# Kernel optimization log

Measured on AMD Instinct MI355X. Metric: run time of the kernel, lower is better.

Reference implementation:

```python
import jax, jax.numpy as jnp
import numpy as np
import math

B, L, C, Hh, Ww = 1, 16, 32, 64, 64
Wf = Ww // 2 + 1
R = 16
GROUPS = 4
MID = 4  # max(C//16, 4)
DT_REF = 1.0
INJ_K = 2.0
EPS = 1e-5


def _conv2d(x, w, b):
    y = jax.lax.conv_general_dilated(x, w, (1, 1), 'SAME',
                                     dimension_numbers=('NCHW', 'OIHW', 'NCHW'))
    return y + b[None, :, None, None]


def _adaptive_avg_w(x, out_w):
    # adaptive avg pool along last axis (torch AdaptiveAvgPool semantics)
    w_in = x.shape[-1]
    cs = jnp.concatenate([jnp.zeros(x.shape[:-1] + (1,), x.dtype), jnp.cumsum(x, -1)], -1)
    starts = np.floor(np.arange(out_w) * w_in / out_w).astype(np.int32)
    ends = np.ceil((np.arange(out_w) + 1) * w_in / out_w).astype(np.int32)
    num = cs[..., ends] - cs[..., starts]
    den = jnp.asarray(ends - starts, x.dtype)
    return num / den


def setup_inputs() -> dict:
    key = jax.random.key(0)
    ks = jax.random.split(key, 24)
    s = 0.05
    inp = {}
    inp['x'] = jax.random.normal(ks[0], (B, C, L, Hh, Ww), jnp.float32)
    inp['dt'] = jax.random.uniform(ks[1], (B, L), jnp.float32, 0.1, 1.0)
    inp['conv1_w'] = jax.random.normal(ks[2], (C, C, 3, 3), jnp.float32) * s
    inp['conv1_b'] = jnp.zeros((C,), jnp.float32)
    inp['conv2_w'] = jax.random.normal(ks[3], (C, C, 3, 3), jnp.float32) * s
    inp['conv2_b'] = jnp.zeros((C,), jnp.float32)
    inp['gfc_w'] = jax.random.normal(ks[4], (C, C), jnp.float32) * s
    inp['gfc_b'] = jnp.zeros((C,), jnp.float32)
    inp['head_w'] = jax.random.normal(ks[5], (C * R * 3, C), jnp.float32) * 0.02
    hb = np.zeros((C, R, 3), np.float32); hb[..., 0] = 1.0; hb[..., 2] = -5.0
    inp['head_b'] = jnp.asarray(hb.reshape(-1))
    inp['mix_w'] = jnp.eye(2 * R, dtype=jnp.float32) + jax.random.normal(ks[6], (2 * R, 2 * R), jnp.float32) * 0.02
    inp['mix_b'] = jnp.zeros((2 * R,), jnp.float32)
    inp['rank_scale'] = jnp.ones((R,), jnp.float32)
    inp['proj_w'] = jax.random.normal(ks[7], (1, R), jnp.float32) * s
    inp['proj_b'] = jnp.zeros((1,), jnp.float32)
    inp['pif_w'] = jax.random.normal(ks[8], (C, C), jnp.float32) * s  # 1x1x1 Conv3d
    inp['pif_b'] = jnp.zeros((C,), jnp.float32)
    inp['gn_w'] = jnp.ones((C,), jnp.float32)
    inp['gn_b'] = jnp.zeros((C,), jnp.float32)
    inp['g1_w'] = jax.random.normal(ks[9], (MID, C), jnp.float32) * s
    inp['g1_b'] = jnp.zeros((MID,), jnp.float32)
    inp['g2_w'] = jax.random.normal(ks[10], (C, MID), jnp.float32) * s
    inp['g2_b'] = jnp.zeros((C,), jnp.float32)
    return inp


def _forward(x, dt, conv1_w, conv1_b, conv2_w, conv2_b, gfc_w, gfc_b, head_w, head_b,
             mix_w, mix_b, rank_scale, proj_w, proj_b, pif_w, pif_b, gn_w, gn_b,
             g1_w, g1_b, g2_w, g2_b):
    Bx, Cx, Lx, H, W = x.shape
    x_seq = jnp.transpose(x, (0, 2, 1, 3, 4))  # [B,L,C,H,W]
    # ---- DynamicsParameterEstimator on flattened [B*L,C,H,W] ----
    xf = x_seq.reshape(Bx * Lx, Cx, H, W)
    f = jax.nn.silu(_conv2d(xf, conv1_w, conv1_b))
    f = jax.nn.silu(_conv2d(f, conv2_w, conv2_b))
    glob = jax.nn.sigmoid(f.mean((2, 3)) @ gfc_w.T + gfc_b)  # [BL,C]
    f = f * glob[:, :, None, None]
    f = _adaptive_avg_w(f.mean(2), Wf)         # [BL,C,Wf]
    feat = jnp.transpose(f, (0, 2, 1))          # [BL,Wf,C]
    p = (feat @ head_w.T + head_b).reshape(Bx * Lx, Wf, Cx, R, 3)
    nu = jax.nn.softplus(p[..., 0]).reshape(Bx, Lx, Wf, Cx, R)
    th = (jnp.tanh(p[..., 1]) * math.pi).reshape(Bx, Lx, Wf, Cx, R)
    sg = jax.nn.sigmoid(p[..., 2]).reshape(Bx, Lx, Wf, Cx, R)
    nu = jnp.transpose(nu, (0, 1, 3, 2, 4))[:, :, :, None]  # [B,L,C,1,Wf,R]
    th = jnp.transpose(th, (0, 1, 3, 2, 4))[:, :, :, None]
    sg = jnp.transpose(sg, (0, 1, 3, 2, 4))[:, :, :, None]
    # ---- Koopman A (triton kernel math): exp(-nu*dt) * exp(i*theta*dt) ----
    dtb = dt[:, :, None, None, None, None]
    decay = jnp.exp(-nu * dtb)
    ang = th * dtb
    A = jax.lax.complex(decay * jnp.cos(ang), decay * jnp.sin(ang))  # [B,L,C,1,Wf,R]
    # ---- injection in rfft space, gated by dt ----
    g = 1.0 - jnp.exp(-INJ_K * jnp.clip(dt / max(DT_REF, 1e-6), 0.0))  # [B,L]
    xfreq = jnp.fft.rfft(x_seq, axis=-1)        # [B,L,C,H,Wf] complex
    u = sg * xfreq[..., None] * g[:, :, None, None, None, None]  # [B,L,C,H,Wf,R]
    # ---- parallel linear recurrence h_t = A_t h_{t-1} + u_t ----
    def combine(a, b):
        Aa, ua = a
        Ab, ub = b
        return (Ab * Aa, Ab * ua + ub)
    _, h = jax.lax.associative_scan(combine, (A, u), axis=1)  # h: [B,L,C,H,Wf,R]
    # ---- SpectralMixer over rank (real/imag stacked) ----
    hs = jnp.concatenate([h.real, h.imag], -1) @ mix_w.T + mix_b
    hr, hi = jnp.split(hs, 2, -1)
    h = jax.lax.complex(hr, hi) * rank_scale
    # ---- rank projection + irfft ----
    y = jnp.einsum('blchfr,r->blchf', h, proj_w[0].astype(h.dtype)) + proj_b[0]
    y = jnp.fft.irfft(y, n=W, axis=-1)          # [B,L,C,H,W]
    y = jnp.transpose(y, (0, 2, 1, 3, 4))        # [B,C,L,H,W]
    # ---- post_ifft_proj: 1x1x1 Conv3d ----
    y = jnp.einsum('bclhw,oc->bolhw', y, pif_w) + pif_b[None, :, None, None, None]
    # ---- SpatialGroupNorm (per-frame GroupNorm, 4 groups) ----
    z = jnp.transpose(y, (0, 2, 1, 3, 4)).reshape(Bx * Lx, GROUPS, (Cx // GROUPS) * H * W)
    mu = z.mean(-1, keepdims=True)
    var = z.var(-1, keepdims=True)
    z = (z - mu) / jnp.sqrt(var + EPS)
    z = z.reshape(Bx, Lx, Cx, H, W) * gn_w[None, None, :, None, None] + gn_b[None, None, :, None, None]
    y = jnp.transpose(z, (0, 2, 1, 3, 4))        # [B,C,L,H,W]
    # ---- LatitudeGating (squeeze-excite over W) ----
    ym = y.mean(-1)                              # [B,C,L,H]
    yg = jnp.transpose(ym, (0, 2, 3, 1))          # [B,L,H,C]
    yg = jax.nn.sigmoid(jax.nn.silu(yg @ g1_w.T + g1_b) @ g2_w.T + g2_b)
    gate = jnp.transpose(yg, (0, 3, 1, 2))[..., None]  # [B,C,L,H,1]
    return x + y * gate


def reference(x, dt, conv1_w, conv1_b, conv2_w, conv2_b, gfc_w, gfc_b, head_w, head_b,
              mix_w, mix_b, rank_scale, proj_w, proj_b, pif_w, pif_b, gn_w, gn_b,
              g1_w, g1_b, g2_w, g2_b):
    return _forward(x, dt, conv1_w, conv1_b, conv2_w, conv2_b, gfc_w, gfc_b, head_w,
                    head_b, mix_w, mix_b, rank_scale, proj_w, proj_b, pif_w, pif_b,
                    gn_w, gn_b, g1_w, g1_b, g2_w, g2_b)
```

## Files before the change

kernel.cpp:

```cpp
#include <hip/hip_runtime.h>
#include <hip/hip_bf16.h>
#include <math.h>

#define CC 32
#define LL 16
#define HH 64
#define WW 64
#define WF 33
#define RR 16
#define PI_F 3.14159265358979323846f

typedef __attribute__((ext_vector_type(8))) short short8;
typedef __attribute__((ext_vector_type(4))) float f32x4;

#define OFF_F1      0
#define OFF_COLSUM  2097152
#define OFF_FEAT    2130944
#define OFF_XFR     2958848
#define OFF_XFI     4040192
#define OFF_YFR     5121536
#define OFF_YFI     6202880
#define OFF_PART    2958848
#define OFF_Y1      2958848
#define OFF_Y2      0
#define OFF_GNM     7284224
#define OFF_GNR     7284288
#define OFF_YM      7284352
#define OFF_GATE    7317120
#define OFF_WVEC    7349888
#define OFF_WT      7350016
#define OFF_YQ      7370496

__device__ __forceinline__ float sigmoidf_(float x){ return 1.0f/(1.0f+expf(-x)); }
__device__ __forceinline__ unsigned short f2bf(float v){
    __hip_bfloat16 b = __float2bfloat16(v);
    return *reinterpret_cast<unsigned short*>(&b);
}
__device__ __forceinline__ float bf2f(unsigned short u){
    __hip_bfloat16 b = *reinterpret_cast<__hip_bfloat16*>(&u);
    return __bfloat162float(b);
}

__global__ void k_prep0(const float* __restrict__ mix_w, const float* __restrict__ mix_b,
                        const float* __restrict__ rank_scale, const float* __restrict__ proj_w,
                        const float* __restrict__ proj_b,
                        const float* __restrict__ c1w, const float* __restrict__ c2w,
                        float* __restrict__ ws){
    unsigned short* wt = (unsigned short*)(ws + OFF_WT);
    if (blockIdx.x == 0){
        float* wv = ws + OFF_WVEC;
        int t = threadIdx.x;
        if (t < 32){
            float sre=0.f, sim=0.f;
            for (int r=0;r<RR;r++){
                float a = proj_w[r]*rank_scale[r];
                sre += a*mix_w[r*2*RR + t];
                sim += a*mix_w[(RR+r)*2*RR + t];
            }
            wv[t] = sre; wv[32+t] = sim;
        }
        if (t == 0){
            float cre=0.f, cim=0.f;
            for (int r=0;r<RR;r++){
                float a = proj_w[r]*rank_scale[r];
                cre += a*mix_b[r];
                cim += a*mix_b[RR+r];
            }
            wv[64] = cre + proj_b[0]; wv[65] = cim;
        }
        return;
    }
    int i = (blockIdx.x-1)*256 + threadIdx.x;
    if (i < 18432){
        int which = (i >= 9216);
        int j = which ? i - 9216 : i;
        int je   = j & 7;
        int lane = (j >> 3) & 63;
        int ct   = (j >> 9) & 1;
        int tap  = j >> 10;
        int kh = tap/3, kw = tap - kh*3;
        int co = ct*16 + (lane & 15);
        int ci = (lane >> 4)*8 + je;
        const float* cw = which ? c2w : c1w;
        wt[i] = f2bf(cw[((co*CC + ci)*3 + kh)*3 + kw]);
        return;
    }
    i -= 18432;
    if (i < 10240){
        int j = i & 7, lane = (i>>3)&63, cch = (i>>9)&3, t = i>>11;
        int frow = t*16 + (lane & 15);
        int k = ((lane>>4)&3)*8 + j;
        int w = (cch & 1)*32 + k;
        float coef = 0.f;
        if (frow < 33)       coef =  cosf(2.0f*PI_F*(float)(frow*w)/64.0f);
        else if (frow < 66)  coef = -sinf(2.0f*PI_F*(float)((frow-33)*w)/64.0f);
        unsigned short hi = f2bf(coef);
        wt[18432 + i] = (cch < 2) ? hi : f2bf(coef - bf2f(hi));
        return;
    }
    i -= 10240;
    if (i < 12288){
        int wtile = i / 3072;
        int rem = i - wtile*3072;
        int ch = rem >> 9;
        int ll = rem & 511;
        int lane = ll >> 3, j = ll & 7;
        int w = wtile*16 + (lane & 15);
        int k = (ch % 3)*32 + ((lane>>4)&3)*8 + j;
        float coef = 0.f;
        if (k < 33){
            float s = (k==0 || k==32) ? 1.f : 2.f;
            coef = s*cosf(2.0f*PI_F*(float)(k*w)/64.0f)*(1.0f/64.0f);
        } else if (k < 66){
            int f = k - 33;
            float s = (f==0 || f==32) ? 1.f : 2.f;
            coef = -s*sinf(2.0f*PI_F*(float)(f*w)/64.0f)*(1.0f/64.0f);
        }
        unsigned short hi = f2bf(coef);
        wt[18432 + 10240 + i] = (ch < 3) ? hi : f2bf(coef - bf2f(hi));
        return;
    }
}

__global__ __launch_bounds__(256, 4) void k_conv1m(const float* __restrict__ x,
                                                   const unsigned short* __restrict__ wt,
                                                   const float* __restrict__ cb,
                                                   unsigned short* __restrict__ f1p){
    __shared__ __align__(16) unsigned short xs[4*66*32];
    __shared__ __align__(16) unsigned short pw[9216];

    const int tid  = threadIdx.x;
    const int l    = blockIdx.x >> 5;
    const int h0   = (blockIdx.x & 31)*2;
    const int wid  = tid >> 6;
    const int lane = tid & 63;
    const int col  = lane & 15;
    const int kgrp = lane >> 4;

    {
        const unsigned int* src = (const unsigned int*)wt;
        unsigned int* dst = (unsigned int*)pw;
        #pragma unroll
        for (int j = 0; j < 18; ++j) dst[tid + j*256] = src[tid + j*256];
    }
    {
        const int rr = tid >> 6;
        const int w  = tid & 63;
        int hh = h0 - 1 + rr;
        bool hv = (hh >= 0 && hh < HH);
        const float* sp = x + (long)l*HH*WW + hh*WW + w;
        int wIdx = 1 + w;
        #pragma unroll
        for (int cib = 0; cib < 4; ++cib){
            float v[8];
            #pragma unroll
            for (int k = 0; k < 8; ++k)
                v[k] = hv ? sp[(long)(cib*8 + k)*LL*HH*WW] : 0.f;
            uint4 p;
            p.x = (unsigned)f2bf(v[0]) | ((unsigned)f2bf(v[1])<<16);
            p.y = (unsigned)f2bf(v[2]) | ((unsigned)f2bf(v[3])<<16);
            p.z = (unsigned)f2bf(v[4]) | ((unsigned)f2bf(v[5])<<16);
            p.w = (unsigned)f2bf(v[6]) | ((unsigned)f2bf(v[7])<<16);
            int cs = cib ^ (wIdx & 3);
            *(uint4*)&xs[(rr*66 + wIdx)*32 + cs*8] = p;
        }
    }
    if (tid < 32){
        int row = tid >> 3, rest = tid & 7;
        int wIdx = (rest >> 2) ? 65 : 0;
        int cib = rest & 3;
        *(uint4*)&xs[(row*66 + wIdx)*32 + cib*8] = make_uint4(0,0,0,0);
    }
    __syncthreads();

    #pragma unroll
    for (int u = 0; u < 4; ++u){
        int unit = wid + u*4;
        int hloc = unit >> 3;
        int rem  = unit & 7;
        int ct   = rem >> 2;
        int wt16 = rem & 3;
        int colw = wt16*16 + col;
        f32x4 acc = {0.f,0.f,0.f,0.f};
        #pragma unroll
        for (int kh = 0; kh < 3; ++kh){
            #pragma unroll
            for (int kw = 0; kw < 3; ++kw){
                int wIdx = colw + kw;
                int cs = kgrp ^ (wIdx & 3);
                short8 b = *(const short8*)&xs[((hloc+kh)*66 + wIdx)*32 + cs*8];
                short8 a = *(const short8*)&pw[((kh*3+kw)*2 + ct)*512 + lane*8];
                acc = __builtin_amdgcn_mfma_f32_16x16x32_bf16(a, b, acc, 0, 0, 0);
            }
        }
        int co0 = ct*16 + kgrp*4;
        int h = h0 + hloc;
        float o[4];
        #pragma unroll
        for (int r = 0; r < 4; ++r){
            float v = acc[r] + cb[co0+r];
            o[r] = v * sigmoidf_(v);
        }
        uint2 pk;
        pk.x = (unsigned)f2bf(o[0]) | ((unsigned)f2bf(o[1])<<16);
        pk.y = (unsigned)f2bf(o[2]) | ((unsigned)f2bf(o[3])<<16);
        *(uint2*)&f1p[(((long)l*HH + h)*WW + colw)*32 + co0] = pk;
    }
}

__global__ __launch_bounds__(256, 4) void k_conv2m(const unsigned short* __restrict__ f1p,
                                                   const unsigned short* __restrict__ wt,
                                                   const float* __restrict__ cb,
                                                   float* __restrict__ ws){
    __shared__ __align__(16) unsigned short xs[4*66*32];
    __shared__ __align__(16) unsigned short pw[9216];

    const int tid  = threadIdx.x;
    const int l    = blockIdx.x >> 5;
    const int h0   = (blockIdx.x & 31)*2;
    const int wid  = tid >> 6;
    const int lane = tid & 63;
    const int col  = lane & 15;
    const int kgrp = lane >> 4;

    {
        const unsigned int* src = (const unsigned int*)wt;
        unsigned int* dst = (unsigned int*)pw;
        #pragma unroll
        for (int j = 0; j < 18; ++j) dst[tid + j*256] = src[tid + j*256];
    }
    {
        const int rr = tid >> 6;
        const int w  = tid & 63;
        int hh = h0 - 1 + rr;
        bool hv = (hh >= 0 && hh < HH);
        const uint4* sp = (const uint4*)&f1p[(((long)l*HH + hh)*WW + w)*32];
        int wIdx = 1 + w;
        #pragma unroll
        for (int cib = 0; cib < 4; ++cib){
            uint4 p = hv ? sp[cib] : make_uint4(0,0,0,0);
            int cs = cib ^ (wIdx & 3);
            *(uint4*)&xs[(rr*66 + wIdx)*32 + cs*8] = p;
        }
    }
    if (tid < 32){
        int row = tid >> 3, rest = tid & 7;
        int wIdx = (rest >> 2) ? 65 : 0;
        int cib = rest & 3;
        *(uint4*)&xs[(row*66 + wIdx)*32 + cib*8] = make_uint4(0,0,0,0);
    }
    __syncthreads();

    #pragma unroll
    for (int u = 0; u < 4; ++u){
        int unit = wid + u*4;
        int hloc = unit >> 3;
        int rem  = unit & 7;
        int ct   = rem >> 2;
        int wt16 = rem & 3;
        int colw = wt16*16 + col;
        f32x4 acc = {0.f,0.f,0.f,0.f};
        #pragma unroll
        for (int kh = 0; kh < 3; ++kh){
            #pragma unroll
            for (int kw = 0; kw < 3; ++kw){
                int wIdx = colw + kw;
                int cs = kgrp ^ (wIdx & 3);
                short8 b = *(const short8*)&xs[((hloc+kh)*66 + wIdx)*32 + cs*8];
                short8 a = *(const short8*)&pw[((kh*3+kw)*2 + ct)*512 + lane*8];
                acc = __builtin_amdgcn_mfma_f32_16x16x32_bf16(a, b, acc, 0, 0, 0);
            }
        }
        int co0 = ct*16 + kgrp*4;
        int h = h0 + hloc;
        float* pp = ws + OFF_PART + ((long)(l*HH + h))*2048 + colw;
        #pragma unroll
        for (int r = 0; r < 4; ++r){
            float v = acc[r] + cb[co0+r];
            pp[(co0+r)*WW] = v * sigmoidf_(v);
        }
    }
}

__global__ void k_colred(float* __restrict__ ws){
    int b = blockIdx.x;
    int l = b >> 5, c = b & 31;
    int w = threadIdx.x;
    const float* p = ws + OFF_PART + (long)l*HH*2048 + c*WW + w;
    float s = 0.f;
    #pragma unroll 8
    for (int h = 0; h < HH; ++h) s += p[h*2048];
    ws[OFF_COLSUM + (l*CC + c)*WW + w] = s;
}

__global__ void k_globfeat(const float* __restrict__ gfc_w, const float* __restrict__ gfc_b,
                           float* __restrict__ ws){
    __shared__ float gs[CC], gl[CC];
    int l = blockIdx.x;
    int tid = threadIdx.x;
    if (tid < 32){
        const float* cs = ws + OFF_COLSUM + (l*CC+tid)*WW;
        float s = 0.f;
        for (int w=0;w<WW;w++) s += cs[w];
        gs[tid] = s;
    }
    __syncthreads();
    if (tid < 32){
        float acc = gfc_b[tid];
        for (int i=0;i<CC;i++) acc += gs[i]*(1.0f/4096.0f)*gfc_w[tid*CC+i];
        gl[tid] = sigmoidf_(acc);
    }
    __syncthreads();
    for (int i = tid; i < WF*CC; i += 256){
        int c = i & 31, wf = i >> 5;
        int s = (wf*64)/33;
        int e = ((wf+1)*64 + 32)/33;
        const float* cs = ws + OFF_COLSUM + (l*CC+c)*WW;
        float sum = 0.f;
        for (int w=s;w<e;w++) sum += cs[w];
        ws[OFF_FEAT + (l*WF+wf)*CC + c] = gl[c] * sum / (64.0f*(float)(e-s));
    }
}

__global__ __launch_bounds__(256, 4) void k_rfftm(const float* __restrict__ x,
                                                  const unsigned short* __restrict__ at,
                                                  float* __restrict__ ws){
    __shared__ __align__(16) unsigned short xs[HH*68];
    __shared__ float fre[33*64];
    __shared__ float fim[33*64];
    int b = blockIdx.x; int l = b >> 5, c = b & 31;
    int tid = threadIdx.x;
    const int wid  = tid >> 6;
    const int lane = tid & 63;
    const int col  = lane & 15;
    const int kgrp = lane >> 4;

    const float* xp = x + (long)(c*LL + l)*HH*WW;
    for (int i = tid; i < HH*WW; i += 256){
        int h = i >> 6, w = i & 63;
        xs[h*68 + w] = f2bf(xp[i]);
    }
    __syncthreads();

    #pragma unroll
    for (int q = 0; q < 5; ++q){
        int unit = wid + q*4;
        int ftile = unit >> 2;
        int htile = unit & 3;
        f32x4 acc = {0.f,0.f,0.f,0.f};
        #pragma unroll
        for (int cch = 0; cch < 4; ++cch){
            short8 a = *(const short8*)&at[(((ftile*4 + cch)*64) + lane)*8];
            short8 bb = *(const short8*)&xs[(htile*16 + col)*68 + (cch & 1)*32 + kgrp*8];
            acc = __builtin_amdgcn_mfma_f32_16x16x32_bf16(a, bb, acc, 0, 0, 0);
        }
        int h = htile*16 + col;
        #pragma unroll
        for (int r = 0; r < 4; ++r){
            int fr = ftile*16 + kgrp*4 + r;
            if (fr < 33)      fre[fr*64 + h] = acc[r];
            else if (fr < 66) fim[(fr-33)*64 + h] = acc[r];
        }
    }
    __syncthreads();
    unsigned* xfp = (unsigned*)(ws + OFF_XFR) + (long)(l*CC + c)*2112;
    for (int i = tid; i < 2112; i += 256){
        xfp[i] = (unsigned)f2bf(fre[i]) | ((unsigned)f2bf(fim[i]) << 16);
    }
}

__global__ __launch_bounds__(256) void k_scan(const float* __restrict__ hw,
                                              const float* __restrict__ hb,
                                              const float* __restrict__ dt,
                                              float* __restrict__ ws){
    __shared__ float lA[LL*RR], lI[LL*RR], lS[LL*RR];
    __shared__ float wv[66];
    __shared__ float lfeat[LL*CC];
    int b = blockIdx.x;
    int c = b / WF, f = b - c*WF;
    int tid = threadIdx.x;
    if (tid < 66) wv[tid] = ws[OFF_WVEC + tid];
    for (int i = tid; i < LL*CC; i += 256){
        int l = i >> 5, ii = i & 31;
        lfeat[i] = ws[OFF_FEAT + (l*WF + f)*CC + ii];
    }
    __syncthreads();
    {
        int l = tid >> 4, r = tid & 15;
        const float* feat = lfeat + l*CC;
        int j0 = (c*RR + r)*3;
        const float* w0 = hw + j0*CC;
        float p0=hb[j0], p1=hb[j0+1], p2=hb[j0+2];
        #pragma unroll 8
        for (int i=0;i<CC;i++){
            float fv = feat[i];
            p0 += fv*w0[i]; p1 += fv*w0[CC+i]; p2 += fv*w0[2*CC+i];
        }
        float nu = fmaxf(p0,0.f) + log1pf(expf(-fabsf(p0)));
        float th = tanhf(p1)*PI_F;
        float sg = sigmoidf_(p2);
        float dtv = dt[l];
        float decay = expf(-nu*dtv);
        float ang = th*dtv;
        lA[tid] = decay*cosf(ang);
        lI[tid] = decay*sinf(ang);
        lS[tid] = sg*(1.0f - expf(-2.0f*fmaxf(dtv,0.f)));
    }
    __syncthreads();
    const int h  = tid >> 2;
    const int rq = tid & 3;
    float sre[4] = {0,0,0,0}, sim[4] = {0,0,0,0};
    float w0_[4], w1_[4], w2_[4], w3_[4];
    #pragma unroll
    for (int q=0;q<4;q++){
        int r = rq*4 + q;
        w0_[q]=wv[r]; w1_[q]=wv[16+r]; w2_[q]=wv[32+r]; w3_[q]=wv[48+r];
    }
    const float cre = wv[64], cim = wv[65];
    const long fh = (long)(c*WF + f)*HH + h;
    const unsigned* xfp = (const unsigned*)(ws + OFF_XFR);
    unsigned* yfp = (unsigned*)(ws + OFF_YFR);
    #pragma unroll 2
    for (int l=0;l<LL;l++){
        unsigned px = xfp[l*(CC*HH*WF) + fh];
        float xr = bf2f((unsigned short)(px & 0xffffu));
        float xi = bf2f((unsigned short)(px >> 16));
        float yr = 0.f, yi = 0.f;
        #pragma unroll
        for (int q=0;q<4;q++){
            int r = rq*4 + q;
            float a = lA[l*16+r], ii = lI[l*16+r], s = lS[l*16+r];
            float nre = a*sre[q] - ii*sim[q] + s*xr;
            float nim = a*sim[q] + ii*sre[q] + s*xi;
            sre[q]=nre; sim[q]=nim;
            yr += w0_[q]*nre + w1_[q]*nim;
            yi += w2_[q]*nre + w3_[q]*nim;
        }
        yr += __shfl_xor(yr, 1); yr += __shfl_xor(yr, 2);
        yi += __shfl_xor(yi, 1); yi += __shfl_xor(yi, 2);
        if (rq == 0){
            yfp[l*(CC*HH*WF) + fh] =
                (unsigned)f2bf(yr + cre) | ((unsigned)f2bf(yi + cim) << 16);
        }
    }
}

__global__ __launch_bounds__(256, 4) void k_irfftm(const unsigned short* __restrict__ btb,
                                                   float* __restrict__ ws){
    __shared__ __align__(16) unsigned short mh[HH*100];
    int b = blockIdx.x; int l = b >> 5, c = b & 31;
    int tid = threadIdx.x;
    const int wid  = tid >> 6;
    const int lane = tid & 63;
    const int col  = lane & 15;
    const int kgrp = lane >> 4;

    const unsigned* yfp = (const unsigned*)(ws + OFF_YFR) + (long)(l*CC + c)*2112;
    for (int i = tid; i < 2112; i += 256){
        unsigned p = yfp[i];
        int f = i >> 6, h = i & 63;
        mh[h*100 + f]      = (unsigned short)(p & 0xffffu);
        mh[h*100 + 33 + f] = (unsigned short)(p >> 16);
    }
    for (int i = tid; i < 64*34; i += 256){
        int h = i / 34, f = 66 + (i - (i/34)*34);
        mh[h*100 + f] = 0;
    }
    __syncthreads();

    float* y1 = ws + OFF_Y1 + (long)(l*CC + c)*HH*WW;
    #pragma unroll
    for (int q = 0; q < 4; ++q){
        int unit = wid + q*4;
        int htile = unit >> 2;
        int wtile = unit & 3;
        f32x4 acc = {0.f,0.f,0.f,0.f};
        #pragma unroll
        for (int ch = 0; ch < 6; ++ch){
            int kof = (ch % 3)*32 + kgrp*8;
            short8 a = *(const short8*)&mh[(htile*16 + col)*100 + kof];
            short8 bb = *(const short8*)&btb[(((wtile*6 + ch)*64) + lane)*8];
            acc = __builtin_amdgcn_mfma_f32_16x16x32_bf16(a, bb, acc, 0, 0, 0);
        }
        int w = wtile*16 + col;
        #pragma unroll
        for (int r = 0; r < 4; ++r){
            int h = htile*16 + kgrp*4 + r;
            y1[h*WW + w] = acc[r];
        }
    }
}

__global__ void k_pif(const float* __restrict__ pw, const float* __restrict__ pb,
                      float* __restrict__ ws){
    __shared__ float row[CC][WW];
    int b = blockIdx.x; int l = b>>6, h = b&63;
    int tid = threadIdx.x;
    for (int k=0;k<8;k++){
        int i = tid + k*256;
        int ci = i>>6, w = i&63;
        row[ci][w] = ws[OFF_Y1 + ((l*CC+ci)*HH + h)*WW + w];
    }
    __syncthreads();
    for (int k=0;k<8;k++){
        int i = tid + k*256;
        int o = i>>6, w = i&63;
        float acc = pb[o];
        #pragma unroll
        for (int ci=0;ci<CC;ci++) acc += pw[o*CC+ci]*row[ci][w];
        ws[OFF_Y2 + ((l*CC+o)*HH + h)*WW + w] = acc;
        float s = acc, q = acc*acc;
        s += __shfl_down(s, 32, 64); q += __shfl_down(q, 32, 64);
        s += __shfl_down(s, 16, 64); q += __shfl_down(q, 16, 64);
        s += __shfl_down(s,  8, 64); q += __shfl_down(q,  8, 64);
        s += __shfl_down(s,  4, 64); q += __shfl_down(q,  4, 64);
        s += __shfl_down(s,  2, 64); q += __shfl_down(q,  2, 64);
        s += __shfl_down(s,  1, 64); q += __shfl_down(q,  1, 64);
        if ((tid & 63) == 0){
            ws[OFF_YM + (l*HH+h)*CC + o] = s*(1.0f/64.0f);
            ws[OFF_YQ + (l*HH+h)*CC + o] = q;
        }
    }
}

__global__ void k_gatel(const float* __restrict__ g1w, const float* __restrict__ g1b,
                        const float* __restrict__ g2w, const float* __restrict__ g2b,
                        const float* __restrict__ gnw, const float* __restrict__ gnb,
                        float* __restrict__ ws){
    __shared__ float mus[4], rsd[4];
    __shared__ float ymn[16][CC+1];
    __shared__ float mid[16][4];
    int blk = blockIdx.x;
    int l = blk >> 2, hq = blk & 3;
    int h0 = hq*16;
    int tid = threadIdx.x;

    {
        int g = tid >> 6, j = tid & 63;
        const float* ymp = ws + OFF_YM + (l*HH + j)*CC + g*8;
        const float* yqp = ws + OFF_YQ + (l*HH + j)*CC + g*8;
        float s = 0.f, q = 0.f;
        #pragma unroll
        for (int cc = 0; cc < 8; ++cc){ s += ymp[cc]; q += yqp[cc]; }
        #pragma unroll
        for (int off = 32; off > 0; off >>= 1){
            s += __shfl_down(s, off, 64);
            q += __shfl_down(q, off, 64);
        }
        if (j == 0){
            float mean = s*(1.0f/512.0f);
            float rstd = rsqrtf(q*(1.0f/32768.0f) - mean*mean + 1e-5f);
            mus[g] = mean; rsd[g] = rstd;
            if (hq == 0){ ws[OFF_GNM + l*4+g] = mean; ws[OFF_GNR + l*4+g] = rstd; }
        }
    }
    __syncthreads();
    for (int i = tid; i < 16*CC; i += 256){
        int hh = i >> 5, cidx = i & 31;
        int g = cidx >> 3;
        ymn[hh][cidx] = (ws[OFF_YM + (l*HH + h0 + hh)*CC + cidx] - mus[g])*rsd[g]*gnw[cidx] + gnb[cidx];
    }
    __syncthreads();
    if (tid < 64){
        int hh = tid >> 2, m = tid & 3;
        float a = g1b[m];
        #pragma unroll 8
        for (int i = 0; i < CC; ++i) a += ymn[hh][i]*g1w[m*CC+i];
        mid[hh][m] = a*sigmoidf_(a);
    }
    __syncthreads();
    for (int i = tid; i < 16*CC; i += 256){
        int hh = i >> 5, cidx = i & 31;
        float a = g2b[cidx];
        #pragma unroll
        for (int m = 0; m < 4; ++m) a += mid[hh][m]*g2w[cidx*4+m];
        ws[OFF_GATE + (l*HH + h0 + hh)*CC + cidx] = sigmoidf_(a);
    }
}

__global__ void k_final(const float* __restrict__ x, float* __restrict__ out,
                        const float* __restrict__ gnw, const float* __restrict__ gnb,
                        const float* __restrict__ ws){
    int t = blockIdx.x*256 + threadIdx.x;
    int n = t*4;
    int h = (n>>6)&63, l = (n>>12)&15, c = n>>16;
    int g = c>>3;
    float mu = ws[OFF_GNM + l*4+g], rstd = ws[OFF_GNR + l*4+g];
    float gw = gnw[c]*rstd, gb = gnb[c] - mu*gnw[c]*rstd;
    float4 z  = *(const float4*)(ws + OFF_Y2 + (((l*CC+c)*HH+h)*WW) + (n&63));
    float  gt = ws[OFF_GATE + (l*HH+h)*CC + c];
    float4 xv = *(const float4*)(x + n);
    float4 o;
    o.x = xv.x + (z.x*gw+gb)*gt; o.y = xv.y + (z.y*gw+gb)*gt;
    o.z = xv.z + (z.z*gw+gb)*gt; o.w = xv.w + (z.w*gw+gb)*gt;
    *(float4*)(out + n) = o;
}

extern "C" void kernel_launch(void* const* d_in, const int* in_sizes, int n_in,
                              void* d_out, int out_size, void* d_ws, size_t ws_size,
                              hipStream_t stream){
    const float* x    = (const float*)d_in[0];
    const float* dt   = (const float*)d_in[1];
    const float* c1w  = (const float*)d_in[2];
    const float* c1b  = (const float*)d_in[3];
    const float* c2w  = (const float*)d_in[4];
    const float* c2b  = (const float*)d_in[5];
    const float* gfcw = (const float*)d_in[6];
    const float* gfcb = (const float*)d_in[7];
    const float* hw   = (const float*)d_in[8];
    const float* hb   = (const float*)d_in[9];
    const float* mixw = (const float*)d_in[10];
    const float* mixb = (const float*)d_in[11];
    const float* rs   = (const float*)d_in[12];
    const float* pjw  = (const float*)d_in[13];
    const float* pjb  = (const float*)d_in[14];
    const float* pifw = (const float*)d_in[15];
    const float* pifb = (const float*)d_in[16];
    const float* gnw  = (const float*)d_in[17];
    const float* gnb  = (const float*)d_in[18];
    const float* g1w  = (const float*)d_in[19];
    const float* g1b  = (const float*)d_in[20];
    const float* g2w  = (const float*)d_in[21];
    const float* g2b  = (const float*)d_in[22];
    float* ws  = (float*)d_ws;
    float* out = (float*)d_out;
    unsigned short* wt  = (unsigned short*)(ws + OFF_WT);
    unsigned short* at  = wt + 18432;
    unsigned short* btb = wt + 18432 + 10240;
    unsigned short* f1p = (unsigned short*)(ws + OFF_F1);

    k_prep0   <<<161,  256, 0, stream>>>(mixw, mixb, rs, pjw, pjb, c1w, c2w, ws);
    k_conv1m  <<<512,  256, 0, stream>>>(x, wt, c1b, f1p);
    k_conv2m  <<<512,  256, 0, stream>>>(f1p, wt + 9216, c2b, ws);
    k_colred  <<<512,  64,  0, stream>>>(ws);
    k_globfeat<<<16,   256, 0, stream>>>(gfcw, gfcb, ws);
    k_rfftm   <<<512,  256, 0, stream>>>(x, at, ws);
    k_scan    <<<1056, 256, 0, stream>>>(hw, hb, dt, ws);
    k_irfftm  <<<512,  256, 0, stream>>>(btb, ws);
    k_pif     <<<1024, 256, 0, stream>>>(pifw, pifb, ws);
    k_gatel   <<<64,   256, 0, stream>>>(g1w, g1b, g2w, g2b, gnw, gnb, ws);
    k_final   <<<2048, 256, 0, stream>>>(x, out, gnw, gnb, ws);
}
```

Baseline: 203.3 us.

## Pre-reduce conv2 rows in-block, fuse column reduction into global feature kernel

conv2 now has each wave compute both output rows of its block and sum them before writing, so the partial buffer holds 32 row-pairs instead of 64 rows. The separate column-reduction kernel is merged into the global-feature kernel, which sums the partials into shared memory with float4 loads, removing one launch and a global round trip. The pointwise conv in k_pif caches each input column in registers and maps one output pixel per thread to cut shared-memory reads. Trade-offs: the fused reduction runs on only 16 blocks, and the per-thread register array raises register pressure.

```diff
diff --git a/kernel.cpp b/kernel.cpp
--- a/kernel.cpp
+++ b/kernel.cpp
@@ -14,12 +14,9 @@
 typedef __attribute__((ext_vector_type(4))) float f32x4;
 
 #define OFF_F1      0
-#define OFF_COLSUM  2097152
 #define OFF_FEAT    2130944
 #define OFF_XFR     2958848
-#define OFF_XFI     4040192
 #define OFF_YFR     5121536
-#define OFF_YFI     6202880
 #define OFF_PART    2958848
 #define OFF_Y1      2958848
 #define OFF_Y2      0
@@ -217,7 +214,8 @@
 
     const int tid  = threadIdx.x;
     const int l    = blockIdx.x >> 5;
-    const int h0   = (blockIdx.x & 31)*2;
+    const int ht   = blockIdx.x & 31;
+    const int h0   = ht*2;
     const int wid  = tid >> 6;
     const int lane = tid & 63;
     const int col  = lane & 15;
@@ -252,54 +250,59 @@
     __syncthreads();
 
     #pragma unroll
-    for (int u = 0; u < 4; ++u){
-        int unit = wid + u*4;
-        int hloc = unit >> 3;
-        int rem  = unit & 7;
+    for (int p = 0; p < 2; ++p){
+        int rem  = wid + p*4;
         int ct   = rem >> 2;
         int wt16 = rem & 3;
         int colw = wt16*16 + col;
-        f32x4 acc = {0.f,0.f,0.f,0.f};
+        f32x4 acc0 = {0.f,0.f,0.f,0.f};
+        f32x4 acc1 = {0.f,0.f,0.f,0.f};
         #pragma unroll
         for (int kh = 0; kh < 3; ++kh){
             #pragma unroll
             for (int kw = 0; kw < 3; ++kw){
                 int wIdx = colw + kw;
                 int cs = kgrp ^ (wIdx & 3);
-                short8 b = *(const short8*)&xs[((hloc+kh)*66 + wIdx)*32 + cs*8];
-                short8 a = *(const short8*)&pw[((kh*3+kw)*2 + ct)*512 + lane*8];
-                acc = __builtin_amdgcn_mfma_f32_16x16x32_bf16(a, b, acc, 0, 0, 0);
+                short8 a  = *(const short8*)&pw[((kh*3+kw)*2 + ct)*512 + lane*8];
+                short8 b0 = *(const short8*)&xs[((0+kh)*66 + wIdx)*32 + cs*8];
+                short8 b1 = *(const short8*)&xs[((1+kh)*66 + wIdx)*32 + cs*8];
+                acc0 = __builtin_amdgcn_mfma_f32_16x16x32_bf16(a, b0, acc0, 0, 0, 0);
+                acc1 = __builtin_amdgcn_mfma_f32_16x16x32_bf16(a, b1, acc1, 0, 0, 0);
             }
         }
         int co0 = ct*16 + kgrp*4;
-        int h = h0 + hloc;
-        float* pp = ws + OFF_PART + ((long)(l*HH + h))*2048 + colw;
+        float* pp = ws + OFF_PART + ((long)(l*32 + ht))*2048 + colw;
         #pragma unroll
         for (int r = 0; r < 4; ++r){
-            float v = acc[r] + cb[co0+r];
-            pp[(co0+r)*WW] = v * sigmoidf_(v);
-        }
-    }
-}
-
-__global__ void k_colred(float* __restrict__ ws){
-    int b = blockIdx.x;
-    int l = b >> 5, c = b & 31;
-    int w = threadIdx.x;
-    const float* p = ws + OFF_PART + (long)l*HH*2048 + c*WW + w;
-    float s = 0.f;
-    #pragma unroll 8
-    for (int h = 0; h < HH; ++h) s += p[h*2048];
-    ws[OFF_COLSUM + (l*CC + c)*WW + w] = s;
-}
-
-__global__ void k_globfeat(const float* __restrict__ gfc_w, const float* __restrict__ gfc_b,
-                           float* __restrict__ ws){
+            float bias = cb[co0+r];
+            float v0 = acc0[r] + bias; v0 = v0 * sigmoidf_(v0);
+            float v1 = acc1[r] + bias; v1 = v1 * sigmoidf_(v1);
+            pp[(co0+r)*WW] = v0 + v1;
+        }
+    }
+}
+
+__global__ void k_colglob(const float* __restrict__ gfc_w, const float* __restrict__ gfc_b,
+                          float* __restrict__ ws){
+    __shared__ float colsum[CC*WW];
     __shared__ float gs[CC], gl[CC];
     int l = blockIdx.x;
     int tid = threadIdx.x;
+    const float4* p4 = (const float4*)(ws + OFF_PART + (long)l*32*2048);
+    #pragma unroll
+    for (int s = 0; s < 2; ++s){
+        int idx = tid + s*256;
+        float4 acc = {0.f,0.f,0.f,0.f};
+        #pragma unroll 8
+        for (int ht = 0; ht < 32; ++ht){
+            float4 v = p4[ht*512 + idx];
+            acc.x += v.x; acc.y += v.y; acc.z += v.z; acc.w += v.w;
+        }
+        *(float4*)&colsum[idx*4] = acc;
+    }
+    __syncthreads();
     if (tid < 32){
-        const float* cs = ws + OFF_COLSUM + (l*CC+tid)*WW;
+        const float* cs = colsum + tid*WW;
         float s = 0.f;
         for (int w=0;w<WW;w++) s += cs[w];
         gs[tid] = s;
@@ -315,7 +318,7 @@
         int c = i & 31, wf = i >> 5;
         int s = (wf*64)/33;
         int e = ((wf+1)*64 + 32)/33;
-        const float* cs = ws + OFF_COLSUM + (l*CC+c)*WW;
+        const float* cs = colsum + c*WW;
         float sum = 0.f;
         for (int w=s;w<e;w++) sum += cs[w];
         ws[OFF_FEAT + (l*WF+wf)*CC + c] = gl[c] * sum / (64.0f*(float)(e-s));
@@ -502,12 +505,16 @@
         row[ci][w] = ws[OFF_Y1 + ((l*CC+ci)*HH + h)*WW + w];
     }
     __syncthreads();
+    const int w = tid & 63;
+    float xv[CC];
+    #pragma unroll
+    for (int ci = 0; ci < CC; ++ci) xv[ci] = row[ci][w];
+    #pragma unroll
     for (int k=0;k<8;k++){
-        int i = tid + k*256;
-        int o = i>>6, w = i&63;
+        int o = (tid>>6) + k*4;
         float acc = pb[o];
         #pragma unroll
-        for (int ci=0;ci<CC;ci++) acc += pw[o*CC+ci]*row[ci][w];
+        for (int ci=0;ci<CC;ci++) acc += pw[o*CC+ci]*xv[ci];
         ws[OFF_Y2 + ((l*CC+o)*HH + h)*WW + w] = acc;
         float s = acc, q = acc*acc;
         s += __shfl_down(s, 32, 64); q += __shfl_down(q, 32, 64);
@@ -632,8 +639,7 @@
     k_prep0   <<<161,  256, 0, stream>>>(mixw, mixb, rs, pjw, pjb, c1w, c2w, ws);
     k_conv1m  <<<512,  256, 0, stream>>>(x, wt, c1b, f1p);
     k_conv2m  <<<512,  256, 0, stream>>>(f1p, wt + 9216, c2b, ws);
-    k_colred  <<<512,  64,  0, stream>>>(ws);
-    k_globfeat<<<16,   256, 0, stream>>>(gfcw, gfcb, ws);
+    k_colglob <<<16,   256, 0, stream>>>(gfcw, gfcb, ws);
     k_rfftm   <<<512,  256, 0, stream>>>(x, at, ws);
     k_scan    <<<1056, 256, 0, stream>>>(hw, hb, dt, ws);
     k_irfftm  <<<512,  256, 0, stream>>>(btb, ws);
```

Result: no change. 200.3 us (-1.5%).
